# Optimization experiments

Measured on AMD Instinct MI355X. Metric: run time of the kernel, lower is better.

## Reference

```python
import jax, jax.numpy as jnp
import numpy as np

PROPAGATION_RANGE = 2
PROP_OUT = PROPAGATION_RANGE - 1  # propagation_out_range


def setup_inputs() -> dict:
    key = jax.random.key(0)
    k1, k2 = jax.random.split(key)
    B, D, H, W = 2, 48, 512, 640
    neighbors = 9
    depth_min = jnp.full((B,), 425.0, dtype=jnp.float32)
    depth_max = jnp.full((B,), 935.0, dtype=jnp.float32)
    # depth samples uniformly inside [depth_min, depth_max]
    u = jax.random.uniform(k1, (B, D, H, W), dtype=jnp.float32)
    depth_sample = depth_min[:, None, None, None] + u * (depth_max - depth_min)[:, None, None, None]
    # per-neighbor weights (2*neighbors channels: far-range then near-range)
    offset = jax.random.uniform(k2, (B, 2 * neighbors, H, W), dtype=jnp.float32) / neighbors
    return {
        "depth_sample": depth_sample,
        "depth_min": depth_min,
        "depth_max": depth_max,
        "offset": offset,
        "patchmatch_interval_scale": 0.025,
        "evaluate_neighbors": neighbors,
    }


def reference(depth_sample, depth_min, depth_max, offset, patchmatch_interval_scale, evaluate_neighbors):
    neighbors = int(evaluate_neighbors)
    B, D, H, W = depth_sample.shape
    k = int(np.sqrt(neighbors))  # square neighborhood side

    # normalized inverse depth in [0, 1]
    inv_min = 1.0 / depth_min  # [B]
    inv_max = 1.0 / depth_max  # [B]
    x = (1.0 / depth_sample - inv_max[:, None, None, None]) / (inv_min - inv_max)[:, None, None, None]

    pad = k // 2 + PROP_OUT
    pad1 = 2 * pad
    xp = jnp.pad(x, ((0, 0), (0, 0), (pad, pad), (pad, pad)), mode="reflect")
    xp1 = jnp.pad(x, ((0, 0), (0, 0), (pad1, pad1), (pad1, pad1)), mode="reflect")

    step = PROP_OUT + 1
    acc = jnp.zeros_like(x)
    for s in range(neighbors):  # small static loop (9 neighbors)
        iy, ix = (s // k) * step, (s % k) * step
        iy1, ix1 = 2 * iy, 2 * ix
        # offset channel broadcasts over the depth dimension
        f1 = offset[:, s, None] * xp1[:, :, iy1:H + iy1, ix1:W + ix1]
        f = offset[:, s + neighbors, None] * xp[:, :, iy:H + iy, ix:W + ix]
        acc = acc + (f + f1) * 0.5

    x1 = jnp.abs(acc - x) / patchmatch_interval_scale
    x1 = jnp.clip(x1, 0.0, 4.0)
    return jax.nn.sigmoid((2.0 - x1) * 2.0)
```

## Files before the change

### kernel.cpp

```cpp
#include <hip/hip_runtime.h>

constexpr int Bc = 2, Dc = 48, Hc = 512, Wc = 640;
constexpr int HWc = Hc * Wc;

constexpr int TW = 64, TH = 16;
constexpr int NT = 512;
constexpr int HALO = 4;
constexpr int SW = TW + 2 * HALO;
constexpr int SH = TH + 2 * HALO;
constexpr int DC = 3;
constexpr int NIT = Dc / DC;
constexpr int PLANE = SW * SH;
constexpr int NVEC = (PLANE / 4) * DC;
constexpr int VPT = (NVEC + NT - 1) / NT;
constexpr int NSCAL = PLANE * DC;
constexpr int SPT = (NSCAL + NT - 1) / NT;

__device__ __forceinline__ int reflect_h(int h) {
    return h < 0 ? -h : (h >= Hc ? 2 * (Hc - 1) - h : h);
}
__device__ __forceinline__ int reflect_w(int w) {
    return w < 0 ? -w : (w >= Wc ? 2 * (Wc - 1) - w : w);
}

__global__ __launch_bounds__(NT, 6) void dw_kernel(
    const float* __restrict__ ds, const float* __restrict__ dmin,
    const float* __restrict__ dmax, const float* __restrict__ off,
    const float* __restrict__ scale_p, float* __restrict__ out)
{
    __shared__ float sx[2][DC * PLANE];

    const int b   = blockIdx.z;
    const int h0  = blockIdx.y * TH;
    const int w0  = blockIdx.x * TW;
    const int tid = threadIdx.x;
    const int tw  = tid & 63;
    const int th  = tid >> 6;

    const float inv_min   = 1.0f / dmin[b];
    const float inv_max   = 1.0f / dmax[b];
    const float invd      = 1.0f / (inv_min - inv_max);
    const float inv_scale = 1.0f / scale_p[0];

    float offF[2][9], offN[2][9];
    #pragma unroll
    for (int px = 0; px < 2; ++px) {
        const float* op = off + (size_t)b * 18 * HWc
                        + (size_t)(h0 + th + px * 8) * Wc + (w0 + tw);
        #pragma unroll
        for (int s = 0; s < 9; ++s) {
            offF[px][s] = op[(size_t)s * HWc];
            offN[px][s] = op[(size_t)(s + 9) * HWc];
        }
    }

    const float* dsb  = ds  + (size_t)b * Dc * HWc;
    float*       outb = out + (size_t)b * Dc * HWc
                            + (size_t)(h0 + th) * Wc + (w0 + tw);

    auto compute = [&](const float* sb, int d0) {
        #pragma unroll
        for (int p = 0; p < DC; ++p) {
            #pragma unroll
            for (int px = 0; px < 2; ++px) {
                const float* base = sb + p * PLANE
                                  + (th + px * 8 + HALO) * SW + (tw + HALO);
                float x0  = base[0];
                float acc = 0.0f;
                #pragma unroll
                for (int s = 0; s < 9; ++s) {
                    const int dy = (s / 3) * 2 - 2;
                    const int dx = (s % 3) * 2 - 2;
                    acc += offN[px][s] * base[dy * SW + dx];
                    acc += offF[px][s] * base[2 * dy * SW + 2 * dx];
                }
                acc *= 0.5f;
                float x1 = fminf(fabsf(acc - x0) * inv_scale, 4.0f);
                float t  = 4.0f - 2.0f * x1;
                outb[(size_t)(d0 + p) * HWc + px * 8 * Wc] =
                    __builtin_amdgcn_rcpf(1.0f + __expf(-t));
            }
        }
    };

    const bool interior = (blockIdx.x > 0) && (blockIdx.x + 1 < gridDim.x);

    if (interior) {
        int vsrc[VPT];
        #pragma unroll
        for (int i = 0; i < VPT; ++i) {
            int vid = tid + i * NT;
            if (vid < NVEC) {
                int p   = vid / (PLANE / 4);
                int rem = vid - p * (PLANE / 4);
                int r   = rem / (SW / 4);
                int j   = rem - r * (SW / 4);
                int hs  = reflect_h(h0 + r - HALO);
                vsrc[i] = p * HWc + hs * Wc + (w0 - HALO + 4 * j);
            } else vsrc[i] = 0;
        }
        float4 pre[VPT];
        auto issue = [&](int d0) {
            const float* dp = dsb + (size_t)d0 * HWc;
            #pragma unroll
            for (int i = 0; i < VPT; ++i) {
                int vid = tid + i * NT;
                if (vid < NVEC) pre[i] = *(const float4*)(dp + vsrc[i]);
            }
        };
        auto commit = [&](float* sb) {
            #pragma unroll
            for (int i = 0; i < VPT; ++i) {
                int vid = tid + i * NT;
                if (vid < NVEC) {
                    float4 v = pre[i], x;
                    x.x = (__builtin_amdgcn_rcpf(v.x) - inv_max) * invd;
                    x.y = (__builtin_amdgcn_rcpf(v.y) - inv_max) * invd;
                    x.z = (__builtin_amdgcn_rcpf(v.z) - inv_max) * invd;
                    x.w = (__builtin_amdgcn_rcpf(v.w) - inv_max) * invd;
                    *(float4*)(sb + vid * 4) = x;
                }
            }
        };
        issue(0);
        commit(sx[0]);
        __syncthreads();
        for (int it = 0; it < NIT; ++it) {
            if (it + 1 < NIT) issue((it + 1) * DC);
            compute(sx[it & 1], it * DC);
            if (it + 1 < NIT) commit(sx[(it + 1) & 1]);
            __syncthreads();
        }
    } else {
        int ssrc[SPT];
        #pragma unroll
        for (int i = 0; i < SPT; ++i) {
            int idx = tid + i * NT;
            if (idx < NSCAL) {
                int p   = idx / PLANE;
                int rem = idx - p * PLANE;
                int r   = rem / SW;
                int c   = rem - r * SW;
                int hs  = reflect_h(h0 + r - HALO);
                int ws  = reflect_w(w0 + c - HALO);
                ssrc[i] = p * HWc + hs * Wc + ws;
            } else ssrc[i] = 0;
        }
        float pre[SPT];
        auto issue = [&](int d0) {
            const float* dp = dsb + (size_t)d0 * HWc;
            #pragma unroll
            for (int i = 0; i < SPT; ++i) {
                int idx = tid + i * NT;
                if (idx < NSCAL) pre[i] = dp[ssrc[i]];
            }
        };
        auto commit = [&](float* sb) {
            #pragma unroll
            for (int i = 0; i < SPT; ++i) {
                int idx = tid + i * NT;
                if (idx < NSCAL)
                    sb[idx] = (__builtin_amdgcn_rcpf(pre[i]) - inv_max) * invd;
            }
        };
        issue(0);
        commit(sx[0]);
        __syncthreads();
        for (int it = 0; it < NIT; ++it) {
            if (it + 1 < NIT) issue((it + 1) * DC);
            compute(sx[it & 1], it * DC);
            if (it + 1 < NIT) commit(sx[(it + 1) & 1]);
            __syncthreads();
        }
    }
}

extern "C" void kernel_launch(void* const* d_in, const int* in_sizes, int n_in,
                              void* d_out, int out_size, void* d_ws, size_t ws_size,
                              hipStream_t stream) {
    const float* ds   = (const float*)d_in[0];
    const float* dmin = (const float*)d_in[1];
    const float* dmax = (const float*)d_in[2];
    const float* off  = (const float*)d_in[3];
    const float* sc   = (const float*)d_in[4];
    float* out = (float*)d_out;

    dim3 grid(Wc / TW, Hc / TH, Bc);
    dw_kernel<<<grid, NT, 0, stream>>>(ds, dmin, dmax, off, sc, out);
}
```

Before: 303.5 us.

## Split depth across blocks and compute four pixels per thread with vector LDS reads

The depth dimension is split into two chunks handled by separate blocks, which doubles the grid to expose more parallelism. Each block now has 256 threads, and each thread computes four adjacent output pixels from five 12-float row loads out of shared memory. Offsets are loaded as float4 and outputs are stored as float4. The aim is to cut LDS load instructions by reusing shared rows across neighbor taps, and to improve occupancy with smaller blocks. In exchange, the halo is loaded twice (once per depth chunk block) and each thread holds more registers for the offset weights.

```diff
diff --git a/kernel.cpp b/kernel.cpp
--- a/kernel.cpp
+++ b/kernel.cpp
@@ -3,18 +3,19 @@
 constexpr int Bc = 2, Dc = 48, Hc = 512, Wc = 640;
 constexpr int HWc = Hc * Wc;
 
-constexpr int TW = 64, TH = 16;
-constexpr int NT = 512;
+constexpr int TW = 64, TH = 16, NT = 256;
 constexpr int HALO = 4;
 constexpr int SW = TW + 2 * HALO;
 constexpr int SH = TH + 2 * HALO;
-constexpr int DC = 3;
-constexpr int NIT = Dc / DC;
 constexpr int PLANE = SW * SH;
-constexpr int NVEC = (PLANE / 4) * DC;
+constexpr int DC = 2;
+constexpr int DSPLIT = 2;
+constexpr int DCHUNK = Dc / DSPLIT;
+constexpr int NIT = DCHUNK / DC;
+constexpr int NVEC = DC * PLANE / 4;
 constexpr int VPT = (NVEC + NT - 1) / NT;
-constexpr int NSCAL = PLANE * DC;
-constexpr int SPT = (NSCAL + NT - 1) / NT;
+constexpr int NSC = DC * PLANE;
+constexpr int SPT = (NSC + NT - 1) / NT;
 
 __device__ __forceinline__ int reflect_h(int h) {
     return h < 0 ? -h : (h >= Hc ? 2 * (Hc - 1) - h : h);
@@ -23,63 +24,89 @@
     return w < 0 ? -w : (w >= Wc ? 2 * (Wc - 1) - w : w);
 }
 
-__global__ __launch_bounds__(NT, 6) void dw_kernel(
+__global__ __launch_bounds__(NT) void dw_kernel(
     const float* __restrict__ ds, const float* __restrict__ dmin,
     const float* __restrict__ dmax, const float* __restrict__ off,
     const float* __restrict__ scale_p, float* __restrict__ out)
 {
     __shared__ float sx[2][DC * PLANE];
 
-    const int b   = blockIdx.z;
-    const int h0  = blockIdx.y * TH;
-    const int w0  = blockIdx.x * TW;
-    const int tid = threadIdx.x;
-    const int tw  = tid & 63;
-    const int th  = tid >> 6;
+    const int bz   = blockIdx.z;
+    const int b    = bz >> 1;
+    const int dch  = bz & 1;
+    const int h0   = blockIdx.y * TH;
+    const int w0   = blockIdx.x * TW;
+    const int tid  = threadIdx.x;
+    const int col4 = tid & 15;
+    const int row  = tid >> 4;
 
     const float inv_min   = 1.0f / dmin[b];
     const float inv_max   = 1.0f / dmax[b];
     const float invd      = 1.0f / (inv_min - inv_max);
     const float inv_scale = 1.0f / scale_p[0];
 
-    float offF[2][9], offN[2][9];
-    #pragma unroll
-    for (int px = 0; px < 2; ++px) {
+    float offF[9][4], offN[9][4];
+    {
         const float* op = off + (size_t)b * 18 * HWc
-                        + (size_t)(h0 + th + px * 8) * Wc + (w0 + tw);
+                        + (size_t)(h0 + row) * Wc + (w0 + 4 * col4);
         #pragma unroll
         for (int s = 0; s < 9; ++s) {
-            offF[px][s] = op[(size_t)s * HWc];
-            offN[px][s] = op[(size_t)(s + 9) * HWc];
+            float4 vF = *(const float4*)(op + (size_t)s * HWc);
+            float4 vN = *(const float4*)(op + (size_t)(s + 9) * HWc);
+            offF[s][0] = vF.x; offF[s][1] = vF.y; offF[s][2] = vF.z; offF[s][3] = vF.w;
+            offN[s][0] = vN.x; offN[s][1] = vN.y; offN[s][2] = vN.z; offN[s][3] = vN.w;
         }
     }
 
-    const float* dsb  = ds  + (size_t)b * Dc * HWc;
+    const float* dsb  = ds  + ((size_t)b * Dc + dch * DCHUNK) * HWc;
     float*       outb = out + (size_t)b * Dc * HWc
-                            + (size_t)(h0 + th) * Wc + (w0 + tw);
-
-    auto compute = [&](const float* sb, int d0) {
+                            + (size_t)(h0 + row) * Wc + (w0 + 4 * col4);
+    const int dg0 = dch * DCHUNK;
+
+    auto compute = [&](const float* sb, int dglob0) {
         #pragma unroll
         for (int p = 0; p < DC; ++p) {
-            #pragma unroll
-            for (int px = 0; px < 2; ++px) {
-                const float* base = sb + p * PLANE
-                                  + (th + px * 8 + HALO) * SW + (tw + HALO);
-                float x0  = base[0];
-                float acc = 0.0f;
-                #pragma unroll
-                for (int s = 0; s < 9; ++s) {
-                    const int dy = (s / 3) * 2 - 2;
-                    const int dx = (s % 3) * 2 - 2;
-                    acc += offN[px][s] * base[dy * SW + dx];
-                    acc += offF[px][s] * base[2 * dy * SW + 2 * dx];
-                }
-                acc *= 0.5f;
-                float x1 = fminf(fabsf(acc - x0) * inv_scale, 4.0f);
+            const float* base = sb + p * PLANE + (row + HALO) * SW + 4 * col4;
+            float acc[4] = {0.f, 0.f, 0.f, 0.f};
+            float x0[4], rb[12];
+            auto ld12 = [&](const float* q) {
+                *(float4*)(rb)     = *(const float4*)(q);
+                *(float4*)(rb + 4) = *(const float4*)(q + 4);
+                *(float4*)(rb + 8) = *(const float4*)(q + 8);
+            };
+            ld12(base - 4 * SW);
+            #pragma unroll
+            for (int j = 0; j < 4; ++j)
+                acc[j] += offF[0][j]*rb[j] + offF[1][j]*rb[j+4] + offF[2][j]*rb[j+8];
+            ld12(base - 2 * SW);
+            #pragma unroll
+            for (int j = 0; j < 4; ++j)
+                acc[j] += offN[0][j]*rb[j+2] + offN[1][j]*rb[j+4] + offN[2][j]*rb[j+6];
+            ld12(base);
+            #pragma unroll
+            for (int j = 0; j < 4; ++j) {
+                x0[j] = rb[j + 4];
+                acc[j] += offN[3][j]*rb[j+2] + offN[4][j]*rb[j+4] + offN[5][j]*rb[j+6]
+                        + offF[3][j]*rb[j]   + offF[4][j]*rb[j+4] + offF[5][j]*rb[j+8];
+            }
+            ld12(base + 2 * SW);
+            #pragma unroll
+            for (int j = 0; j < 4; ++j)
+                acc[j] += offN[6][j]*rb[j+2] + offN[7][j]*rb[j+4] + offN[8][j]*rb[j+6];
+            ld12(base + 4 * SW);
+            #pragma unroll
+            for (int j = 0; j < 4; ++j)
+                acc[j] += offF[6][j]*rb[j] + offF[7][j]*rb[j+4] + offF[8][j]*rb[j+8];
+
+            float4 o; float* po = (float*)&o;
+            #pragma unroll
+            for (int j = 0; j < 4; ++j) {
+                float a  = 0.5f * acc[j];
+                float x1 = fminf(fabsf(a - x0[j]) * inv_scale, 4.0f);
                 float t  = 4.0f - 2.0f * x1;
-                outb[(size_t)(d0 + p) * HWc + px * 8 * Wc] =
-                    __builtin_amdgcn_rcpf(1.0f + __expf(-t));
-            }
+                po[j] = __builtin_amdgcn_rcpf(1.0f + __expf(-t));
+            }
+            *(float4*)(outb + (size_t)(dglob0 + p) * HWc) = o;
         }
     };
 
@@ -127,7 +154,7 @@
         __syncthreads();
         for (int it = 0; it < NIT; ++it) {
             if (it + 1 < NIT) issue((it + 1) * DC);
-            compute(sx[it & 1], it * DC);
+            compute(sx[it & 1], dg0 + it * DC);
             if (it + 1 < NIT) commit(sx[(it + 1) & 1]);
             __syncthreads();
         }
@@ -136,7 +163,7 @@
         #pragma unroll
         for (int i = 0; i < SPT; ++i) {
             int idx = tid + i * NT;
-            if (idx < NSCAL) {
+            if (idx < NSC) {
                 int p   = idx / PLANE;
                 int rem = idx - p * PLANE;
                 int r   = rem / SW;
@@ -152,14 +179,14 @@
             #pragma unroll
             for (int i = 0; i < SPT; ++i) {
                 int idx = tid + i * NT;
-                if (idx < NSCAL) pre[i] = dp[ssrc[i]];
+                if (idx < NSC) pre[i] = dp[ssrc[i]];
             }
         };
         auto commit = [&](float* sb) {
             #pragma unroll
             for (int i = 0; i < SPT; ++i) {
                 int idx = tid + i * NT;
-                if (idx < NSCAL)
+                if (idx < NSC)
                     sb[idx] = (__builtin_amdgcn_rcpf(pre[i]) - inv_max) * invd;
             }
         };
@@ -168,7 +195,7 @@
         __syncthreads();
         for (int it = 0; it < NIT; ++it) {
             if (it + 1 < NIT) issue((it + 1) * DC);
-            compute(sx[it & 1], it * DC);
+            compute(sx[it & 1], dg0 + it * DC);
             if (it + 1 < NIT) commit(sx[(it + 1) & 1]);
             __syncthreads();
         }
@@ -185,6 +212,6 @@
     const float* sc   = (const float*)d_in[4];
     float* out = (float*)d_out;
 
-    dim3 grid(Wc / TW, Hc / TH, Bc);
+    dim3 grid(Wc / TW, Hc / TH, Bc * DSPLIT);
     dw_kernel<<<grid, NT, 0, stream>>>(ds, dmin, dmax, off, sc, out);
 }
```

Result: faster. 270.4 us (-10.9%).
